# Performance work log

Hardware: AMD Instinct MI355X
Metric: run time of the kernel (lower is better)

Reference implementation:

```python
import jax, jax.numpy as jnp
import numpy as np

EPS = 1e-7
INF = 1e8
SOFT_CENTER_RADIUS = 3.0
TOPK = 13
IOU_WEIGHT = 3.0
NUM_CLASSES = 80
N_PRIORS = 33600
NUM_GT = 256
IMG = 1024.0


def setup_inputs() -> dict:
    key = jax.random.key(0)
    k1, k2, k3, k4, k5, k6, k7 = jax.random.split(key, 7)
    n, g, c = N_PRIORS, NUM_GT, NUM_CLASSES
    pred_scores = jax.random.normal(k1, (n, c), jnp.float32)
    # priors: (cx, cy, stride, stride)
    ctr = jax.random.uniform(k2, (n, 2), jnp.float32) * IMG
    stride = jnp.full((n, 1), 8.0, jnp.float32)
    priors = jnp.concatenate([ctr, stride, stride], axis=-1)
    # predicted boxes, x1y1x2y2
    pwh = jax.random.uniform(k3, (n, 2), jnp.float32) * 96.0 + 8.0
    pctr = jax.random.uniform(k4, (n, 2), jnp.float32) * IMG
    pred_bboxes = jnp.concatenate([pctr - pwh / 2, pctr + pwh / 2], axis=-1)
    # gt boxes, x1y1x2y2
    gwh = jax.random.uniform(k5, (g, 2), jnp.float32) * 192.0 + 16.0
    gctr = jax.random.uniform(k6, (g, 2), jnp.float32) * IMG
    gt_bboxes = jnp.concatenate([gctr - gwh / 2, gctr + gwh / 2], axis=-1)
    gt_labels = jax.random.randint(k7, (g,), 0, c, dtype=jnp.int32).astype(jnp.int64)
    return {"pred_scores": pred_scores, "priors": priors,
            "pred_bboxes": pred_bboxes, "gt_bboxes": gt_bboxes,
            "gt_labels": gt_labels}


def _pairwise_iou(a, b):
    # a: (n,4), b: (g,4), x1y1x2y2 -> (n,g)
    area_a = (a[:, 2] - a[:, 0]) * (a[:, 3] - a[:, 1])
    area_b = (b[:, 2] - b[:, 0]) * (b[:, 3] - b[:, 1])
    lt = jnp.maximum(a[:, None, :2], b[None, :, :2])
    rb = jnp.minimum(a[:, None, 2:], b[None, :, 2:])
    wh = jnp.clip(rb - lt, 0.0, None)
    inter = wh[..., 0] * wh[..., 1]
    union = area_a[:, None] + area_b[None, :] - inter
    return inter / jnp.maximum(union, 1e-6)


def reference(pred_scores, priors, pred_bboxes, gt_bboxes, gt_labels):
    n, g = pred_bboxes.shape[0], gt_bboxes.shape[0]
    gt_labels = gt_labels.astype(jnp.int32)

    # ---- find_inside_points (box_dim == 4) ----
    pts = priors[:, :2]                                   # (n,2)
    lt = pts[:, None, :] - gt_bboxes[None, :, :2]
    rb = gt_bboxes[None, :, 2:] - pts[:, None, :]
    is_in_gts = jnp.min(jnp.concatenate([lt, rb], -1), -1) > 0   # (n,g)
    pad_bbox_flag = gt_bboxes.sum(-1) > 0                        # (g,)
    is_in_gts = is_in_gts & pad_bbox_flag[None, :]
    valid_mask = jnp.any(is_in_gts, -1)                          # (n,)

    # ---- soft center prior ----
    gt_center = (gt_bboxes[:, :2] + gt_bboxes[:, 2:]) * 0.5      # (g,2)
    dist = jnp.sqrt(((pts[:, None, :] - gt_center[None, :, :]) ** 2).sum(-1))
    dist = dist / priors[:, 2:3]                                 # / stride
    dist = dist * valid_mask[:, None].astype(dist.dtype)
    soft_center_prior = jnp.power(10.0, dist - SOFT_CENTER_RADIUS)

    # ---- iou cost ----
    ious = _pairwise_iou(pred_bboxes, gt_bboxes)                 # (n,g)
    iou_cost = -jnp.log(ious + EPS) * IOU_WEIGHT

    # ---- soft classification cost (BCE-with-logits, iou targets) ----
    logits = pred_scores[:, gt_labels]                           # (n,g)
    scale = jnp.abs(ious - jax.nn.sigmoid(logits)) ** 2
    bce = jnp.maximum(logits, 0) - logits * ious + jnp.log1p(jnp.exp(-jnp.abs(logits)))
    cost = bce * scale + iou_cost + soft_center_prior
    cost = jnp.where(valid_mask[:, None], cost, INF)

    # ---- dynamic k matching (vectorized over GTs) ----
    K = min(TOPK, n)
    topk_ious, _ = jax.lax.top_k(ious.T, K)                      # (g,K)
    dynamic_ks = jnp.clip(topk_ious.sum(-1).astype(jnp.int32), 1, None)  # (g,)
    _, cand_idx = jax.lax.top_k(-cost.T, K)                      # (g,K) lowest-cost priors per gt
    sel = (jnp.arange(K)[None, :] < dynamic_ks[:, None]).astype(jnp.float32)
    matching = jnp.zeros((g, n), jnp.float32).at[
        jnp.arange(g)[:, None], cand_idx].set(sel).T             # (n,g)

    # resolve priors matched to multiple gts -> keep min-cost gt
    multi = matching.sum(-1) > 1
    onehot_min = jax.nn.one_hot(jnp.argmin(cost, -1), g, dtype=jnp.float32)
    matching = jnp.where(multi[:, None], onehot_min, matching)

    fg = matching.sum(-1) > 0
    matched_gt_inds = jnp.argmax(matching, -1)                   # (n,)
    matched_pred_ious = (matching * ious).sum(-1)                # (n,)

    final = fg & valid_mask
    assigned_gt_inds = jnp.where(final, matched_gt_inds + 1, 0)
    assigned_labels = jnp.where(final, gt_labels[matched_gt_inds], -1)
    max_overlaps = jnp.where(final, matched_pred_ious, -INF)
    return assigned_gt_inds, max_overlaps, assigned_labels
```

## Files before the change

### kernel.cpp

```cpp
#include <hip/hip_runtime.h>
#include <cstdint>

#define NPRI 33600
#define NGT  256
#define NCLS 80
#define KTOP 13
#define INF_F 1.0e8f
#define EPS_F 1e-7f
#define L10 3.3219280948873623f
#define SLC  4
#define SLEN (NPRI / SLC)
#define SCN_T 512
#define NW8 (SCN_T / 64)
#define NIT  ((SLEN + SCN_T - 1) / SCN_T)
#define CAPI 1536
#define CAPC 512
#define RFIX 5.5f
#define PREP_BLKS ((NPRI + 255) / 256)
#define NEGINF __int_as_float(0xff800000)

typedef unsigned long long u64;

__device__ __forceinline__ int get_label(const void* p, int j, int is64) {
    if (is64) return (int)((const long long*)p)[j];
    return ((const int*)p)[j];
}

__device__ __forceinline__ float wave_max_bc_f32(float v) {
    #pragma unroll
    for (int off = 32; off > 0; off >>= 1) v = fmaxf(v, __shfl_down(v, off, 64));
    return __int_as_float(__builtin_amdgcn_readfirstlane(__float_as_int(v)));
}
__device__ __forceinline__ u64 wave_min_bc_u64(u64 v) {
    #pragma unroll
    for (int off = 32; off > 0; off >>= 1) { u64 o = __shfl_down(v, off, 64); v = (o < v) ? o : v; }
    unsigned lo = (unsigned)__builtin_amdgcn_readfirstlane((int)(v & 0xffffffffull));
    unsigned hi = (unsigned)__builtin_amdgcn_readfirstlane((int)(v >> 32));
    return (((u64)hi) << 32) | lo;
}
template<int NSL>
__device__ __forceinline__ void wave_merge_max13_f32(float (&l)[NSL], float* dst, int lane) {
    int p = 0;
    for (int r = 0; r < KTOP; ++r) {
        float cur = NEGINF;
        #pragma unroll
        for (int s = 0; s < NSL; ++s) if (s == p) cur = l[NSL - 1 - s];
        float bm = wave_max_bc_f32(cur);
        u64 m = __ballot(cur == bm && bm != NEGINF);
        int first = __ffsll(m) - 1;
        if (lane == first) p++;
        if (lane == 0) dst[r] = bm;
    }
}
template<int NSL>
__device__ __forceinline__ void wave_merge_minN(u64 (&l)[NSL], u64* dst, int lane) {
    int p = 0;
    for (int r = 0; r < KTOP; ++r) {
        u64 cur = ~0ull;
        #pragma unroll
        for (int s = 0; s < NSL; ++s) if (s == p) cur = l[s];
        u64 bm = wave_min_bc_u64(cur);
        if (cur == bm && bm != ~0ull) p++;
        if (lane == 0) dst[r] = bm;
    }
}

__device__ __forceinline__ float iou_exact(float4 pb, float areap, float gx1, float gy1,
                                           float gx2, float gy2, float areag) {
    float iw = fmaxf(fminf(pb.z, gx2) - fmaxf(pb.x, gx1), 0.0f);
    float ih = fmaxf(fminf(pb.w, gy2) - fmaxf(pb.y, gy1), 0.0f);
    float inter = iw * ih;
    return inter / fmaxf(areap + areag - inter, 1e-6f);
}
__device__ __forceinline__ float cost_exact(float4 p2, float gcx, float gcy,
                                            float l, float iou) {
    float dx = p2.x - gcx, dy = p2.y - gcy;
    float dist = sqrtf(dx * dx + dy * dy) / p2.z;
    float soft = exp2f((dist - 3.0f) * L10);
    float sig = 1.0f / (1.0f + expf(-l));
    float dd = iou - sig;
    float bce = fmaxf(l, 0.0f) - l * iou + log1pf(expf(-fabsf(l)));
    float iouc = -logf(iou + EPS_F) * 3.0f;
    return bce * (dd * dd) + iouc + soft;
}

__global__ __launch_bounds__(256) void k_prep(
        const float* __restrict__ priors, const float* __restrict__ gt,
        const void* labels, const float* __restrict__ pboxes,
        float4* __restrict__ pbp,
        int* count, int* firstgt, int* flag, int* nmulti) {
    __shared__ float4 gbox[NGT];
    __shared__ int    gpad[NGT];
    __shared__ int    bad;
    const int tid = threadIdx.x;
    const int b = blockIdx.x;
    if (b == 0 && tid == 0) { bad = 0; *nmulti = 0; }
    {
        float4 bx = ((const float4*)gt)[tid];
        gbox[tid] = bx;
        gpad[tid] = ((bx.x + bx.y + bx.z + bx.w) > 0.0f) ? 1 : 0;
    }
    __syncthreads();
    if (b == 0 && tid < 128) {
        long long v = ((const long long*)labels)[tid];
        if (v < 0 || v >= NCLS) atomicOr(&bad, 1);
    }
    int i = b * 256 + tid;
    if (i < NPRI) {
        count[i] = 0; firstgt[i] = NGT;
        float4 pr = ((const float4*)priors)[i];
        float px = pr.x, py = pr.y;
        int v = 0;
        for (int j = 0; j < NGT; ++j) {
            float4 bx = gbox[j];
            float m = fminf(fminf(px - bx.x, py - bx.y), fminf(bx.z - px, bx.w - py));
            if (m > 0.0f && gpad[j]) { v = 1; break; }
        }
        pbp[2 * i]     = ((const float4*)pboxes)[i];
        pbp[2 * i + 1] = make_float4(px, py, pr.z, v ? 1.0f : 0.0f);
    }
    if (b == 0) {
        __syncthreads();
        if (tid == 0) *flag = bad ? 0 : 1;
    }
}

__global__ __launch_bounds__(SCN_T) void k_scan(
        const float* __restrict__ scores,
        const float4* __restrict__ pbp,
        const float* __restrict__ gt, const void* labels, const int* flag,
        float* __restrict__ part_iou, u64* __restrict__ part_cost) {
    const int tid = threadIdx.x, lane = tid & 63, wid = tid >> 6;
    const int j = blockIdx.x, slice = blockIdx.y;
    const int base = slice * SLEN;
    const int is64 = *flag;

    const float4 gb = ((const float4*)gt)[j];
    const float gx1 = gb.x, gy1 = gb.y, gx2 = gb.z, gy2 = gb.w;
    const float areag = (gx2 - gx1) * (gy2 - gy1);
    const float gcx = (gx1 + gx2) * 0.5f, gcy = (gy1 + gy2) * 0.5f;
    const int lab = get_label(labels, j, is64);

    __shared__ int s_ni, s_nc, s_mode;
    __shared__ float s_dmax;
    __shared__ float liou[CAPI];
    __shared__ int lcost[CAPC];
    __shared__ float wiof[NW8 * KTOP];
    __shared__ u64 wco[NW8 * KTOP];
    __shared__ u64 csel[KTOP];
    if (tid == 0) { s_ni = 0; s_nc = 0; }
    __syncthreads();

    for (int it = 0; it < NIT; ++it) {
        int i = base + tid + it * SCN_T;
        bool inb = (i < base + SLEN);
        float iou = 0.0f;
        bool pc = false;
        if (inb) {
            float4 pb = pbp[2 * i];
            float4 p2 = pbp[2 * i + 1];
            float areap = (pb.z - pb.x) * (pb.w - pb.y);
            float iw = fmaxf(fminf(pb.z, gx2) - fmaxf(pb.x, gx1), 0.0f);
            float ih = fmaxf(fminf(pb.w, gy2) - fmaxf(pb.y, gy1), 0.0f);
            float inter = iw * ih;
            iou = inter / fmaxf(areap + areag - inter, 1e-6f);
            if (p2.w != 0.0f) {
                float dx = p2.x - gcx, dy = p2.y - gcy;
                float rad = p2.z * RFIX;
                pc = (dx * dx + dy * dy <= rad * rad * (1.0f + 1e-5f));
            }
        }
        bool pi = inb && (iou > 0.0f);
        u64 mi = __ballot(pi);
        if (mi) {
            int lead = __ffsll(mi) - 1;
            int cnt = __popcll(mi);
            int bs = 0;
            if (lane == lead) bs = atomicAdd(&s_ni, cnt);
            bs = __shfl(bs, lead, 64);
            if (pi) {
                int p = bs + __popcll(mi & ((1ull << lane) - 1ull));
                if (p < CAPI) liou[p] = iou;
            }
        }
        u64 mc = __ballot(pc);
        if (mc) {
            int lead = __ffsll(mc) - 1;
            int cnt = __popcll(mc);
            int bs = 0;
            if (lane == lead) bs = atomicAdd(&s_nc, cnt);
            bs = __shfl(bs, lead, 64);
            if (pc) {
                int p = bs + __popcll(mc & ((1ull << lane) - 1ull));
                if (p < CAPC) lcost[p] = i;
            }
        }
    }
    __syncthreads();
    const int ni = s_ni, nc = s_nc;
    const int ncc = (nc < CAPC) ? nc : CAPC;
    const bool fI = (ni > CAPI);

    if (wid == 0) {
        u64 lf[KTOP];
        #pragma unroll
        for (int s = 0; s < KTOP; ++s) lf[s] = ~0ull;
        for (int k = lane; k < ncc; k += 64) {
            int i = lcost[k];
            float4 pb = pbp[2 * i];
            float4 p2 = pbp[2 * i + 1];
            float areap = (pb.z - pb.x) * (pb.w - pb.y);
            float iou = iou_exact(pb, areap, gx1, gy1, gx2, gy2, areag);
            float ec = cost_exact(p2, gcx, gcy, scores[(size_t)i * NCLS + lab], iou);
            u64 ck = (((u64)__float_as_uint(ec)) << 32) | (unsigned)i;
            if (ck < lf[KTOP - 1]) {
                lf[KTOP - 1] = ck;
                #pragma unroll
                for (int s = KTOP - 1; s > 0; --s)
                    if (lf[s] < lf[s - 1]) { u64 t = lf[s]; lf[s] = lf[s - 1]; lf[s - 1] = t; }
            }
        }
        wave_merge_minN<KTOP>(lf, csel, lane);
        if (lane == 0) {
            u64 tk = csel[KTOP - 1];
            int mode; float dmax = 0.0f;
            if (tk == ~0ull) mode = 2;
            else {
                float tau = __uint_as_float((unsigned)(tk >> 32));
                if (!(tau < 9.0e7f)) mode = 2;
                else {
                    dmax = 3.0f + __log2f(tau + 1e-5f) * (1.0f / L10) + 4e-3f;
                    mode = (dmax > RFIX || nc > CAPC) ? 1 : 0;
                }
            }
            s_mode = mode; s_dmax = dmax;
        }
    } else if (wid == 1 && !fI) {
        float lf[KTOP];
        #pragma unroll
        for (int s = 0; s < KTOP; ++s) lf[s] = NEGINF;
        int nn = (ni < CAPI) ? ni : CAPI;
        for (int k = lane; k < nn; k += 64) {
            float v = liou[k];
            if (v > lf[0]) {
                lf[0] = v;
                #pragma unroll
                for (int s = 0; s < KTOP - 1; ++s)
                    if (lf[s] > lf[s + 1]) { float t = lf[s]; lf[s] = lf[s + 1]; lf[s + 1] = t; }
            }
        }
        wave_merge_max13_f32<KTOP>(lf, part_iou + ((size_t)j * SLC + slice) * KTOP, lane);
    }
    __syncthreads();

    if (fI) {
        float lf[KTOP];
        #pragma unroll
        for (int s = 0; s < KTOP; ++s) lf[s] = NEGINF;
        for (int i = base + tid; i < base + SLEN; i += SCN_T) {
            float4 pb = pbp[2 * i];
            float areap = (pb.z - pb.x) * (pb.w - pb.y);
            float iou = iou_exact(pb, areap, gx1, gy1, gx2, gy2, areag);
            if (iou > lf[0]) {
                lf[0] = iou;
                #pragma unroll
                for (int s = 0; s < KTOP - 1; ++s)
                    if (lf[s] > lf[s + 1]) { float t = lf[s]; lf[s] = lf[s + 1]; lf[s + 1] = t; }
            }
        }
        wave_merge_max13_f32<KTOP>(lf, &wiof[wid * KTOP], lane);
        __syncthreads();
        if (wid == 0) {
            float* dpi = part_iou + ((size_t)j * SLC + slice) * KTOP;
            int p = 0;
            for (int r = 0; r < KTOP; ++r) {
                float cur = (lane < NW8 && p < KTOP) ? wiof[lane * KTOP + p] : NEGINF;
                float bm = wave_max_bc_f32(cur);
                u64 m = __ballot(cur == bm && bm != NEGINF);
                int first = __ffsll(m) - 1;
                if (lane == first) p++;
                if (lane == 0) dpi[r] = bm;
            }
        }
        __syncthreads();
    }

    int mode = s_mode;
    if (mode == 1) {
        const float dmax = s_dmax;
        if (tid == 0) s_nc = 0;
        __syncthreads();
        for (int i = base + tid; i < base + SLEN; i += SCN_T) {
            float4 p2 = pbp[2 * i + 1];
            if (p2.w != 0.0f) {
                float dx = p2.x - gcx, dy = p2.y - gcy;
                float rad = p2.z * dmax;
                if (dx * dx + dy * dy <= rad * rad * (1.0f + 1e-5f)) {
                    int p = atomicAdd(&s_nc, 1);
                    if (p < CAPC) lcost[p] = i;
                }
            }
        }
        __syncthreads();
        int nc2 = s_nc;
        if (nc2 <= CAPC) {
            if (wid == 0) {
                u64 lf[KTOP];
                #pragma unroll
                for (int s = 0; s < KTOP; ++s) lf[s] = ~0ull;
                for (int k = lane; k < nc2; k += 64) {
                    int i = lcost[k];
                    float4 pb = pbp[2 * i];
                    float4 p2 = pbp[2 * i + 1];
                    float areap = (pb.z - pb.x) * (pb.w - pb.y);
                    float iou = iou_exact(pb, areap, gx1, gy1, gx2, gy2, areag);
                    float ec = cost_exact(p2, gcx, gcy, scores[(size_t)i * NCLS + lab], iou);
                    u64 ck = (((u64)__float_as_uint(ec)) << 32) | (unsigned)i;
                    if (ck < lf[KTOP - 1]) {
                        lf[KTOP - 1] = ck;
                        #pragma unroll
                        for (int s = KTOP - 1; s > 0; --s)
                            if (lf[s] < lf[s - 1]) { u64 t = lf[s]; lf[s] = lf[s - 1]; lf[s - 1] = t; }
                    }
                }
                wave_merge_minN<KTOP>(lf, csel, lane);
            }
        } else {
            mode = 2;
        }
        __syncthreads();
    }
    if (mode == 2) {
        u64 lf[KTOP];
        #pragma unroll
        for (int s = 0; s < KTOP; ++s) lf[s] = ~0ull;
        for (int i = base + tid; i < base + SLEN; i += SCN_T) {
            float4 pb = pbp[2 * i];
            float4 p2 = pbp[2 * i + 1];
            float areap = (pb.z - pb.x) * (pb.w - pb.y);
            float iou = iou_exact(pb, areap, gx1, gy1, gx2, gy2, areag);
            float ec = INF_F;
            if (p2.w != 0.0f) ec = cost_exact(p2, gcx, gcy, scores[(size_t)i * NCLS + lab], iou);
            u64 k2 = (((u64)__float_as_uint(ec)) << 32) | (unsigned)i;
            if (k2 < lf[KTOP - 1]) {
                lf[KTOP - 1] = k2;
                #pragma unroll
                for (int s = KTOP - 1; s > 0; --s)
                    if (lf[s] < lf[s - 1]) { u64 t = lf[s]; lf[s] = lf[s - 1]; lf[s - 1] = t; }
            }
        }
        wave_merge_minN<KTOP>(lf, &wco[wid * KTOP], lane);
        __syncthreads();
        if (wid == 0) {
            int p = 0;
            for (int r = 0; r < KTOP; ++r) {
                u64 cur = (lane < NW8 && p < KTOP) ? wco[lane * KTOP + p] : ~0ull;
                u64 bm = wave_min_bc_u64(cur);
                if (cur == bm && bm != ~0ull) p++;
                if (lane == 0) csel[r] = bm;
            }
        }
        __syncthreads();
    }
    if (tid < KTOP) {
        u64* dpc = part_cost + ((size_t)j * SLC + slice) * KTOP;
        dpc[tid] = csel[tid];
    }
}

__global__ __launch_bounds__(64) void k_merge(
        const float* __restrict__ part_iou, const u64* __restrict__ part_cost,
        int* count, int* firstgt) {
    const int j = blockIdx.x;
    const int lane = threadIdx.x;
    float vi = (lane < SLC * KTOP) ? part_iou[(size_t)j * SLC * KTOP + lane] : NEGINF;
    float tsum = 0.0f;
    for (int r = 0; r < KTOP; ++r) {
        float bm = wave_max_bc_f32(vi);
        u64 m = __ballot(vi == bm && bm != NEGINF);
        int first = __ffsll(m) - 1;
        if (lane == first) vi = NEGINF;
        tsum += (bm == NEGINF) ? 0.0f : bm;
    }
    int ks = (int)tsum;
    if (ks < 1) ks = 1;
    u64 kc = (lane < SLC * KTOP) ? part_cost[(size_t)j * SLC * KTOP + lane] : ~0ull;
    u64 mine = ~0ull;
    for (int r = 0; r < KTOP; ++r) {
        u64 bm = wave_min_bc_u64(kc);
        if (kc == bm && bm != ~0ull) kc = ~0ull;
        if (lane == r) mine = bm;
    }
    if (lane < KTOP && lane < ks && mine != ~0ull) {
        int idx = (int)(unsigned)(mine & 0xFFFFFFFFull);
        atomicAdd(&count[idx], 1);
        atomicMin(&firstgt[idx], j);
    }
}

__global__ __launch_bounds__(256) void k_assign(
        const float4* __restrict__ pbp, const float* __restrict__ gt,
        const void* labels, const int* flag,
        const int* __restrict__ count, const int* __restrict__ firstgt,
        int* nmulti, int* mlist, float* __restrict__ out) {
    __shared__ float4 gbox[NGT];
    __shared__ int glab[NGT];
    __shared__ float gareas[NGT];
    int tid = threadIdx.x;
    int is64 = *flag;
    {
        float4 b = ((const float4*)gt)[tid];
        gbox[tid] = b;
        glab[tid] = get_label(labels, tid, is64);
        gareas[tid] = (b.z - b.x) * (b.w - b.y);
    }
    __syncthreads();
    int i = blockIdx.x * 256 + tid;
    if (i >= NPRI) return;
    float4 p2 = pbp[2 * i + 1];
    int v = (p2.w != 0.0f) ? 1 : 0;
    int c = count[i];
    float o0 = 0.0f, o1 = -INF_F, o2 = -1.0f;
    if (v && c == 1) {
        int j = firstgt[i];
        float4 pb = pbp[2 * i];
        float areap = (pb.z - pb.x) * (pb.w - pb.y);
        float4 g = gbox[j];
        float iw = fmaxf(fminf(pb.z, g.z) - fmaxf(pb.x, g.x), 0.0f);
        float ih = fmaxf(fminf(pb.w, g.w) - fmaxf(pb.y, g.y), 0.0f);
        float inter = iw * ih;
        float iou = inter / fmaxf(areap + gareas[j] - inter, 1e-6f);
        o0 = (float)(j + 1); o1 = iou; o2 = (float)glab[j];
    } else if (v && c > 1) {
        int pos = atomicAdd(nmulti, 1);
        mlist[pos] = i;
    }
    out[i] = o0;
    out[NPRI + i] = o1;
    out[2 * NPRI + i] = o2;
}

__global__ __launch_bounds__(256) void k_multi(
        const float* __restrict__ scores,
        const float4* __restrict__ pbp, const float* __restrict__ gt,
        const void* labels, const int* flag,
        const int* __restrict__ nmulti, const int* __restrict__ mlist,
        float* __restrict__ out) {
    __shared__ float4 gbox[NGT];
    __shared__ int glab[NGT];
    __shared__ float gcxs[NGT], gcys[NGT], gareas[NGT];
    __shared__ u64 red4[4];
    const int tid = threadIdx.x;
    const int is64 = *flag;
    {
        float4 b = ((const float4*)gt)[tid];
        gbox[tid] = b;
        glab[tid] = get_label(labels, tid, is64);
        gcxs[tid] = (b.x + b.z) * 0.5f;
        gcys[tid] = (b.y + b.w) * 0.5f;
        gareas[tid] = (b.z - b.x) * (b.w - b.y);
    }
    __syncthreads();
    const int nm = *nmulti;
    const int j = tid;
    for (int m = blockIdx.x; m < nm; m += gridDim.x) {
        const int i = mlist[m];
        float4 pb = pbp[2 * i];
        float4 p2 = pbp[2 * i + 1];
        float areap = (pb.z - pb.x) * (pb.w - pb.y);

        float4 g = gbox[j];
        float iw = fmaxf(fminf(pb.z, g.z) - fmaxf(pb.x, g.x), 0.0f);
        float ih = fmaxf(fminf(pb.w, g.w) - fmaxf(pb.y, g.y), 0.0f);
        float inter = iw * ih;
        float iou = inter / fmaxf(areap + gareas[j] - inter, 1e-6f);
        float dx = p2.x - gcxs[j], dy = p2.y - gcys[j];
        float dist = sqrtf(dx * dx + dy * dy) / p2.z;
        float soft = exp2f((dist - 3.0f) * L10);
        float l = scores[(size_t)i * NCLS + glab[j]];
        float sig = 1.0f / (1.0f + expf(-l));
        float dd = iou - sig;
        float bce = fmaxf(l, 0.0f) - l * iou + log1pf(expf(-fabsf(l)));
        float cost = bce * (dd * dd) + (-logf(iou + EPS_F) * 3.0f) + soft;

        u64 key = (((u64)__float_as_uint(cost)) << 32) | (unsigned)j;
        u64 v = key;
        #pragma unroll
        for (int off = 32; off > 0; off >>= 1) {
            u64 o = __shfl_down(v, off, 64);
            v = (o < v) ? o : v;
        }
        if ((tid & 63) == 0) red4[tid >> 6] = v;
        __syncthreads();
        u64 best = red4[0];
        #pragma unroll
        for (int q = 1; q < 4; ++q) best = (red4[q] < best) ? red4[q] : best;
        if (key == best) {
            out[i] = (float)(j + 1);
            out[NPRI + i] = iou;
            out[2 * NPRI + i] = (float)glab[j];
        }
        __syncthreads();
    }
}

extern "C" void kernel_launch(void* const* d_in, const int* in_sizes, int n_in,
                              void* d_out, int out_size, void* d_ws, size_t ws_size,
                              hipStream_t stream) {
    const float* scores = (const float*)d_in[0];
    const float* priors = (const float*)d_in[1];
    const float* pboxes = (const float*)d_in[2];
    const float* gt     = (const float*)d_in[3];
    const void*  labels = d_in[4];
    float* out = (float*)d_out;

    char* ws = (char*)d_ws;
    size_t off = 0;
    auto alloc = [&](size_t bytes) { size_t o = off; off = (off + bytes + 255) & ~(size_t)255; return o; };
    int*    flag     = (int*)(ws + alloc(4));
    int*    nmulti   = (int*)(ws + alloc(4));
    int*    count    = (int*)(ws + alloc((size_t)NPRI * 4));
    int*    firstgt  = (int*)(ws + alloc((size_t)NPRI * 4));
    int*    mlist    = (int*)(ws + alloc((size_t)NPRI * 4));
    float*  part_iou = (float*)(ws + alloc((size_t)NGT * SLC * KTOP * 4));
    u64*    part_cost= (u64*)(ws + alloc((size_t)NGT * SLC * KTOP * 8));
    float4* pbp      = (float4*)(ws + alloc((size_t)NPRI * 32));
    (void)ws_size;

    hipLaunchKernelGGL(k_prep, dim3(PREP_BLKS), dim3(256), 0, stream,
                       priors, gt, labels, pboxes, pbp, count, firstgt, flag, nmulti);
    hipLaunchKernelGGL(k_scan, dim3(NGT, SLC), dim3(SCN_T), 0, stream,
                       scores, pbp, gt, labels, flag, part_iou, part_cost);
    hipLaunchKernelGGL(k_merge, dim3(NGT), dim3(64), 0, stream,
                       part_iou, part_cost, count, firstgt);
    hipLaunchKernelGGL(k_assign, dim3((NPRI + 255) / 256), dim3(256), 0, stream,
                       pbp, gt, labels, flag, count, firstgt, nmulti, mlist, out);
    hipLaunchKernelGGL(k_multi, dim3(256), dim3(256), 0, stream,
                       scores, pbp, gt, labels, flag, nmulti, mlist, out);
}
```

Measured before the change: 160.2 us.

## Double prior slices, prefetch next iteration in scan, rework partial merge

Raises the number of prior slices per GT from 4 to 8 so k_scan launches twice as many blocks, each scanning half as many priors. The scan loop now software-prefetches the next iteration's box data into registers so loads overlap with the current iteration's compute. k_merge now has 104 partial candidates per GT, more than one 64-lane wave holds, so it loads two per lane and reuses the existing wave merge helpers to produce the top-13 IoU and cost lists. The trade-off is more partial results and merge work, plus more per-block overhead and shared-memory init against better occupancy.

```diff
diff --git a/kernel.cpp b/kernel.cpp
--- a/kernel.cpp
+++ b/kernel.cpp
@@ -8,7 +8,7 @@
 #define INF_F 1.0e8f
 #define EPS_F 1e-7f
 #define L10 3.3219280948873623f
-#define SLC  4
+#define SLC  8
 #define SLEN (NPRI / SLC)
 #define SCN_T 512
 #define NW8 (SCN_T / 64)
@@ -133,6 +133,7 @@
     const int tid = threadIdx.x, lane = tid & 63, wid = tid >> 6;
     const int j = blockIdx.x, slice = blockIdx.y;
     const int base = slice * SLEN;
+    const int lim = base + SLEN;
     const int is64 = *flag;
 
     const float4 gb = ((const float4*)gt)[j];
@@ -151,49 +152,58 @@
     if (tid == 0) { s_ni = 0; s_nc = 0; }
     __syncthreads();
 
-    for (int it = 0; it < NIT; ++it) {
-        int i = base + tid + it * SCN_T;
-        bool inb = (i < base + SLEN);
-        float iou = 0.0f;
-        bool pc = false;
-        if (inb) {
-            float4 pb = pbp[2 * i];
-            float4 p2 = pbp[2 * i + 1];
-            float areap = (pb.z - pb.x) * (pb.w - pb.y);
-            float iw = fmaxf(fminf(pb.z, gx2) - fmaxf(pb.x, gx1), 0.0f);
-            float ih = fmaxf(fminf(pb.w, gy2) - fmaxf(pb.y, gy1), 0.0f);
-            float inter = iw * ih;
-            iou = inter / fmaxf(areap + areag - inter, 1e-6f);
-            if (p2.w != 0.0f) {
-                float dx = p2.x - gcx, dy = p2.y - gcy;
-                float rad = p2.z * RFIX;
-                pc = (dx * dx + dy * dy <= rad * rad * (1.0f + 1e-5f));
-            }
-        }
-        bool pi = inb && (iou > 0.0f);
-        u64 mi = __ballot(pi);
-        if (mi) {
-            int lead = __ffsll(mi) - 1;
-            int cnt = __popcll(mi);
-            int bs = 0;
-            if (lane == lead) bs = atomicAdd(&s_ni, cnt);
-            bs = __shfl(bs, lead, 64);
-            if (pi) {
-                int p = bs + __popcll(mi & ((1ull << lane) - 1ull));
-                if (p < CAPI) liou[p] = iou;
-            }
-        }
-        u64 mc = __ballot(pc);
-        if (mc) {
-            int lead = __ffsll(mc) - 1;
-            int cnt = __popcll(mc);
-            int bs = 0;
-            if (lane == lead) bs = atomicAdd(&s_nc, cnt);
-            bs = __shfl(bs, lead, 64);
-            if (pc) {
-                int p = bs + __popcll(mc & ((1ull << lane) - 1ull));
-                if (p < CAPC) lcost[p] = i;
-            }
+    {
+        int i = base + tid;
+        float4 pb = pbp[2 * i];
+        float4 p2 = pbp[2 * i + 1];
+        for (int it = 0; it < NIT; ++it) {
+            int inext = i + SCN_T;
+            bool nin = (it + 1 < NIT) && (inext < lim);
+            float4 nb = make_float4(0.f, 0.f, 0.f, 0.f);
+            float4 n2 = make_float4(0.f, 0.f, 0.f, 0.f);
+            if (nin) { nb = pbp[2 * inext]; n2 = pbp[2 * inext + 1]; }
+
+            bool inb = (i < lim);
+            float iou = 0.0f;
+            bool pc = false;
+            if (inb) {
+                float areap = (pb.z - pb.x) * (pb.w - pb.y);
+                float iw = fmaxf(fminf(pb.z, gx2) - fmaxf(pb.x, gx1), 0.0f);
+                float ih = fmaxf(fminf(pb.w, gy2) - fmaxf(pb.y, gy1), 0.0f);
+                float inter = iw * ih;
+                iou = inter / fmaxf(areap + areag - inter, 1e-6f);
+                if (p2.w != 0.0f) {
+                    float dx = p2.x - gcx, dy = p2.y - gcy;
+                    float rad = p2.z * RFIX;
+                    pc = (dx * dx + dy * dy <= rad * rad * (1.0f + 1e-5f));
+                }
+            }
+            bool pi = inb && (iou > 0.0f);
+            u64 mi = __ballot(pi);
+            if (mi) {
+                int lead = __ffsll(mi) - 1;
+                int cnt = __popcll(mi);
+                int bs = 0;
+                if (lane == lead) bs = atomicAdd(&s_ni, cnt);
+                bs = __shfl(bs, lead, 64);
+                if (pi) {
+                    int p = bs + __popcll(mi & ((1ull << lane) - 1ull));
+                    if (p < CAPI) liou[p] = iou;
+                }
+            }
+            u64 mc = __ballot(pc);
+            if (mc) {
+                int lead = __ffsll(mc) - 1;
+                int cnt = __popcll(mc);
+                int bs = 0;
+                if (lane == lead) bs = atomicAdd(&s_nc, cnt);
+                bs = __shfl(bs, lead, 64);
+                if (pc) {
+                    int p = bs + __popcll(mc & ((1ull << lane) - 1ull));
+                    if (p < CAPC) lcost[p] = i;
+                }
+            }
+            i = inext; pb = nb; p2 = n2;
         }
     }
     __syncthreads();
@@ -257,7 +267,7 @@
         float lf[KTOP];
         #pragma unroll
         for (int s = 0; s < KTOP; ++s) lf[s] = NEGINF;
-        for (int i = base + tid; i < base + SLEN; i += SCN_T) {
+        for (int i = base + tid; i < lim; i += SCN_T) {
             float4 pb = pbp[2 * i];
             float areap = (pb.z - pb.x) * (pb.w - pb.y);
             float iou = iou_exact(pb, areap, gx1, gy1, gx2, gy2, areag);
@@ -290,7 +300,7 @@
         const float dmax = s_dmax;
         if (tid == 0) s_nc = 0;
         __syncthreads();
-        for (int i = base + tid; i < base + SLEN; i += SCN_T) {
+        for (int i = base + tid; i < lim; i += SCN_T) {
             float4 p2 = pbp[2 * i + 1];
             if (p2.w != 0.0f) {
                 float dx = p2.x - gcx, dy = p2.y - gcy;
@@ -334,7 +344,7 @@
         u64 lf[KTOP];
         #pragma unroll
         for (int s = 0; s < KTOP; ++s) lf[s] = ~0ull;
-        for (int i = base + tid; i < base + SLEN; i += SCN_T) {
+        for (int i = base + tid; i < lim; i += SCN_T) {
             float4 pb = pbp[2 * i];
             float4 p2 = pbp[2 * i + 1];
             float areap = (pb.z - pb.x) * (pb.w - pb.y);
@@ -373,28 +383,35 @@
         int* count, int* firstgt) {
     const int j = blockIdx.x;
     const int lane = threadIdx.x;
-    float vi = (lane < SLC * KTOP) ? part_iou[(size_t)j * SLC * KTOP + lane] : NEGINF;
+    __shared__ float tiou[KTOP];
+    __shared__ u64 cfin[KTOP];
+
+    float a = (lane < SLC * KTOP) ? part_iou[(size_t)j * SLC * KTOP + lane] : NEGINF;
+    float b = (lane + 64 < SLC * KTOP) ? part_iou[(size_t)j * SLC * KTOP + lane + 64] : NEGINF;
+    float l2[2] = { fminf(a, b), fmaxf(a, b) };
+    wave_merge_max13_f32<2>(l2, tiou, lane);
+
+    u64 ka = (lane < SLC * KTOP) ? part_cost[(size_t)j * SLC * KTOP + lane] : ~0ull;
+    u64 kb = (lane + 64 < SLC * KTOP) ? part_cost[(size_t)j * SLC * KTOP + lane + 64] : ~0ull;
+    u64 c2[2] = { (ka < kb) ? ka : kb, (ka < kb) ? kb : ka };
+    wave_merge_minN<2>(c2, cfin, lane);
+    __syncthreads();
+
     float tsum = 0.0f;
+    #pragma unroll
     for (int r = 0; r < KTOP; ++r) {
-        float bm = wave_max_bc_f32(vi);
-        u64 m = __ballot(vi == bm && bm != NEGINF);
-        int first = __ffsll(m) - 1;
-        if (lane == first) vi = NEGINF;
-        tsum += (bm == NEGINF) ? 0.0f : bm;
+        float v = tiou[r];
+        tsum += (v == NEGINF) ? 0.0f : v;
     }
     int ks = (int)tsum;
     if (ks < 1) ks = 1;
-    u64 kc = (lane < SLC * KTOP) ? part_cost[(size_t)j * SLC * KTOP + lane] : ~0ull;
-    u64 mine = ~0ull;
-    for (int r = 0; r < KTOP; ++r) {
-        u64 bm = wave_min_bc_u64(kc);
-        if (kc == bm && bm != ~0ull) kc = ~0ull;
-        if (lane == r) mine = bm;
-    }
-    if (lane < KTOP && lane < ks && mine != ~0ull) {
-        int idx = (int)(unsigned)(mine & 0xFFFFFFFFull);
-        atomicAdd(&count[idx], 1);
-        atomicMin(&firstgt[idx], j);
+    if (lane < KTOP && lane < ks) {
+        u64 mine = cfin[lane];
+        if (mine != ~0ull) {
+            int idx = (int)(unsigned)(mine & 0xFFFFFFFFull);
+            atomicAdd(&count[idx], 1);
+            atomicMin(&firstgt[idx], j);
+        }
     }
 }
 
```

Measured after the change: 189.1 us. 1.18x slower.
